# Kernel tuning notes

Hardware: AMD Instinct MI355X
Metric: run time of the kernel (lower is better)

The kernel has to match this reference:

```python
import jax, jax.numpy as jnp
import numpy as np
from jax import lax

STRIDE = 16
SCALES = (8.0, 16.0, 32.0)
RATIOS = (0.5, 1.0, 2.0)
PRE_NMS = 6000
POST_NMS = 300
NMS_THRESH = 0.7
MIN_SIZE = 16.0
DN = ('NCHW', 'OIHW', 'NCHW')


def _base_anchors():
    # 9 base anchors centered at (STRIDE/2, STRIDE/2), (ymin,xmin,ymax,xmax)
    c = STRIDE / 2.0
    rows = []
    for r in RATIOS:
        for s in SCALES:
            h = STRIDE * s * np.sqrt(r)
            w = STRIDE * s * np.sqrt(1.0 / r)
            rows.append([c - h / 2, c - w / 2, c + h / 2, c + w / 2])
    return jnp.asarray(np.array(rows, np.float32))


def _all_anchors(wdim, hdim):
    # shift base anchors over the (w, h) feature grid, matching permute(0,2,3,1) flatten order
    sy = jnp.arange(wdim, dtype=jnp.float32) * STRIDE
    sx = jnp.arange(hdim, dtype=jnp.float32) * STRIDE
    yy, xx = jnp.meshgrid(sy, sx, indexing='ij')
    shifts = jnp.stack([yy, xx, yy, xx], axis=-1).reshape(-1, 4)  # [w*h, 4]
    return (shifts[:, None, :] + _base_anchors()[None, :, :]).reshape(-1, 4)  # [w*h*9, 4]


def _conv(x, W, b, pad):
    y = lax.conv_general_dilated(x, W, (1, 1), pad, dimension_numbers=DN)
    return y + b[None, :, None, None]


def _nms_fixed(boxes, keep):
    # sequential greedy NMS over score-sorted boxes; returns POST_NMS boxes (zero padded)
    y1, x1, y2, x2 = boxes[:, 0], boxes[:, 1], boxes[:, 2], boxes[:, 3]
    areas = (y2 - y1) * (x2 - x1)
    N = boxes.shape[0]
    idxs = jnp.arange(N)

    def body(i, keep):
        yy1 = jnp.maximum(y1[i], y1)
        xx1 = jnp.maximum(x1[i], x1)
        yy2 = jnp.minimum(y2[i], y2)
        xx2 = jnp.minimum(x2[i], x2)
        inter = jnp.maximum(yy2 - yy1, 0.0) * jnp.maximum(xx2 - xx1, 0.0)
        iou = inter / (areas[i] + areas - inter + 1e-12)
        suppress = (iou > NMS_THRESH) & (idxs > i) & keep[i]
        return keep & ~suppress

    keep = lax.fori_loop(0, N, body, keep)
    rank = jnp.cumsum(keep) - 1
    slot = jnp.where(keep & (rank < POST_NMS), rank, POST_NMS)  # overflow slot
    out = jnp.zeros((POST_NMS + 1, 4), boxes.dtype).at[slot].set(boxes)
    return out[:POST_NMS]


def _proposals(loc, score_fg, anchors, img_h, img_w):
    ah = anchors[:, 2] - anchors[:, 0]
    aw = anchors[:, 3] - anchors[:, 1]
    acy = anchors[:, 0] + 0.5 * ah
    acx = anchors[:, 1] + 0.5 * aw
    cy = loc[:, 0] * ah + acy
    cx = loc[:, 1] * aw + acx
    h = jnp.exp(loc[:, 2]) * ah
    w = jnp.exp(loc[:, 3]) * aw
    boxes = jnp.stack([cy - 0.5 * h, cx - 0.5 * w, cy + 0.5 * h, cx + 0.5 * w], axis=-1)
    hi = jnp.array([img_h, img_w, img_h, img_w], dtype=boxes.dtype)
    boxes = jnp.clip(boxes, 0.0, hi)
    hs = boxes[:, 2] - boxes[:, 0]
    ws = boxes[:, 3] - boxes[:, 1]
    valid = (hs >= MIN_SIZE) & (ws >= MIN_SIZE)
    sc = jnp.where(valid, score_fg, -jnp.inf)
    top_sc, top_idx = lax.top_k(sc, PRE_NMS)
    cand = boxes[top_idx]
    return _nms_fixed(cand, jnp.isfinite(top_sc))


def setup_inputs() -> dict:
    key = jax.random.key(0)
    k = jax.random.split(key, 4)
    return {
        'base_feature_map': jax.random.normal(k[0], (8, 512, 50, 50), jnp.float32),
        'W_conv': jax.random.normal(k[1], (512, 512, 3, 3), jnp.float32) * 0.01,
        'b_conv': jnp.zeros((512,), jnp.float32),
        'W_cls': jax.random.normal(k[2], (18, 512, 1, 1), jnp.float32) * 0.01,
        'b_cls': jnp.zeros((18,), jnp.float32),
        'W_reg': jax.random.normal(k[3], (36, 512, 1, 1), jnp.float32) * 0.01,
        'b_reg': jnp.zeros((36,), jnp.float32),
        'img_h': 800,
        'img_w': 800,
    }


def reference(base_feature_map, W_conv, b_conv, W_cls, b_cls, W_reg, b_reg, img_h, img_w):
    n, _, w, h = base_feature_map.shape
    anchors = _all_anchors(w, h)  # [w*h*9, 4]
    x = jax.nn.relu(_conv(base_feature_map, W_conv, b_conv, 'SAME'))
    rpn_locs = _conv(x, W_reg, b_reg, 'VALID').transpose(0, 2, 3, 1).reshape(n, -1, 4)
    rpn_scores = _conv(x, W_cls, b_cls, 'VALID').transpose(0, 2, 3, 1).reshape(n, -1, 2)
    fg = jax.nn.softmax(rpn_scores[0], axis=-1)[:, 1]
    rois = _proposals(rpn_locs[0], fg, anchors, float(img_h), float(img_w))
    return rpn_locs, rpn_scores, anchors, rois
```

## Files before the change

### kernel.cpp

```cpp
#include <hip/hip_runtime.h>
#include <cstdint>
#include <math.h>

typedef unsigned int u32;
typedef unsigned long long u64;
typedef __attribute__((ext_vector_type(8))) short short8v;
typedef __attribute__((ext_vector_type(4))) float f32x4;

#define N_BATCH 8
#define C_IN    512
#define PX      2500
#define KDIM    4608
#define NA      22500
#define PRE_NMS 6000
#define POST_NMS 300

#define OUT_SCORES 720000
#define OUT_ANCH   1080000
#define OUT_ROIS   1170000

#define WS_X     0
#define WS_SCORE 10240000
#define WS_BOX   10262500
#define WS_WP    10388608
#define WS_XP    12747904
#define WS_END   22987904

#define NW_ELEMS (512 * KDIM)
#define NX_ELEMS (N_BATCH * C_IN * PX)

__device__ inline u32 rne_hi16(float f) {
    u32 u = __float_as_uint(f);
    return (u + 0x7FFFu + ((u >> 16) & 1u)) >> 16;
}
__device__ inline u32 pack_split(float f) {
    u32 rh  = rne_hi16(f);
    float d = f - __uint_as_float(rh << 16);
    u32 rl  = rne_hi16(d);
    return (rh << 16) | rl;
}

__global__ __launch_bounds__(256) void k_prep(const float* __restrict__ Wc,
                                              const float* __restrict__ in,
                                              u32* __restrict__ WP,
                                              u32* __restrict__ XP) {
    int o = blockIdx.x * 256 + threadIdx.x;
    if (o < NW_ELEMS) {
        int ci_in = o & 31;
        int tmp   = o >> 5;
        int r     = tmp % 9;
        int cc    = tmp / 9;
        int co    = cc >> 4;
        int cig   = cc & 15;
        int ci    = cig * 32 + ci_in;
        WP[o] = pack_split(Wc[(size_t)co * KDIM + ci * 9 + r]);
    } else {
        int o2 = o - NW_ELEMS;
        if (o2 < NX_ELEMS && XP) XP[o2] = pack_split(in[o2]);
    }
}

__global__ __launch_bounds__(256) void k_conv3(const float* __restrict__ in,
                                               const u32* __restrict__ XP,
                                               const u32* __restrict__ WP,
                                               const float* __restrict__ bc,
                                               float* __restrict__ xout) {
    __shared__ unsigned short AsH[128][40];
    __shared__ unsigned short AsL[128][40];
    __shared__ unsigned short BsH[128][40];
    __shared__ unsigned short BsL[128][40];

    int b  = blockIdx.x;
    int n  = b & 7;
    int q  = b >> 3;
    int cb = q & 3;
    int pt = q >> 2;
    int t  = threadIdx.x;
    int lane = t & 63;
    int w  = t >> 6;
    int wr = w >> 1, wc = w & 1;
    int px0 = pt * 128, co0 = cb * 128;
    const float* inN = in + (size_t)n * C_IN * PX;
    const u32*   XPn = XP ? (XP + (size_t)n * C_IN * PX) : nullptr;

    int sco = t >> 1;
    int skb = (t & 1) << 4;
    int spx = t & 127;
    int skk = (t >> 7) << 4;
    int gpx = px0 + spx;
    int sy  = gpx / 50;
    int sx  = gpx - sy * 50;
    bool pxok = (gpx < PX);
    const u32* wpA = WP + (size_t)(co0 + sco) * KDIM + skb;

    f32x4 acc[4][4];
#pragma unroll
    for (int i = 0; i < 4; ++i)
#pragma unroll
        for (int j = 0; j < 4; ++j) acc[i][j] = (f32x4)0.f;

    const int ro = lane & 15;
    const int g8 = (lane >> 4) << 3;

    for (int cig = 0; cig < 16; ++cig) {
        int ci0 = cig << 5;
        for (int r = 0; r < 9; ++r) {
            int kstep = cig * 9 + r;
            {
                const u32* wp = wpA + kstep * 32;
                u32 uu[16];
                *(uint4*)&uu[0]  = *(const uint4*)(wp);
                *(uint4*)&uu[4]  = *(const uint4*)(wp + 4);
                *(uint4*)&uu[8]  = *(const uint4*)(wp + 8);
                *(uint4*)&uu[12] = *(const uint4*)(wp + 12);
                short8v v0, v1, u0, u1;
#pragma unroll
                for (int e = 0; e < 8; ++e) {
                    v0[e] = (short)(uu[e] >> 16);
                    v1[e] = (short)(uu[8 + e] >> 16);
                    u0[e] = (short)(uu[e] & 0xFFFFu);
                    u1[e] = (short)(uu[8 + e] & 0xFFFFu);
                }
                *(short8v*)&AsH[sco][skb]     = v0;
                *(short8v*)&AsH[sco][skb + 8] = v1;
                *(short8v*)&AsL[sco][skb]     = u0;
                *(short8v*)&AsL[sco][skb + 8] = u1;
            }
            {
                int ry = (r * 11) >> 5;
                int dy = ry - 1;
                int dx = r - ry * 3 - 1;
                int iy = sy + dy, ix = sx + dx;
                bool valid = pxok && ((unsigned)iy < 50u) && ((unsigned)ix < 50u);
                int off = iy * 50 + ix;
                short8v v0, v1, u0, u1;
                if (XPn) {
                    const u32* bp = XPn + (size_t)(ci0 + skk) * PX + off;
                    u32 uu[16];
#pragma unroll
                    for (int it = 0; it < 16; ++it)
                        uu[it] = valid ? bp[it * PX] : 0u;
#pragma unroll
                    for (int e = 0; e < 8; ++e) {
                        v0[e] = (short)(uu[e] >> 16);
                        v1[e] = (short)(uu[8 + e] >> 16);
                        u0[e] = (short)(uu[e] & 0xFFFFu);
                        u1[e] = (short)(uu[8 + e] & 0xFFFFu);
                    }
                } else {
                    const float* bp = inN + (size_t)(ci0 + skk) * PX + off;
                    float bv[16];
#pragma unroll
                    for (int it = 0; it < 16; ++it)
                        bv[it] = valid ? bp[it * PX] : 0.f;
#pragma unroll
                    for (int e = 0; e < 8; ++e) {
                        u32 pa = pack_split(bv[e]);
                        u32 pb = pack_split(bv[8 + e]);
                        v0[e] = (short)(pa >> 16);
                        v1[e] = (short)(pb >> 16);
                        u0[e] = (short)(pa & 0xFFFFu);
                        u1[e] = (short)(pb & 0xFFFFu);
                    }
                }
                *(short8v*)&BsH[spx][skk]     = v0;
                *(short8v*)&BsH[spx][skk + 8] = v1;
                *(short8v*)&BsL[spx][skk]     = u0;
                *(short8v*)&BsL[spx][skk + 8] = u1;
            }
            __syncthreads();

            short8v aH[4], aL[4], bH[4], bL[4];
#pragma unroll
            for (int s = 0; s < 4; ++s) {
                aH[s] = *(const short8v*)&AsH[wr * 64 + s * 16 + ro][g8];
                aL[s] = *(const short8v*)&AsL[wr * 64 + s * 16 + ro][g8];
                bH[s] = *(const short8v*)&BsH[wc * 64 + s * 16 + ro][g8];
                bL[s] = *(const short8v*)&BsL[wc * 64 + s * 16 + ro][g8];
            }
#pragma unroll
            for (int i = 0; i < 4; ++i)
#pragma unroll
                for (int j = 0; j < 4; ++j) {
                    acc[i][j] = __builtin_amdgcn_mfma_f32_16x16x32_bf16(aH[i], bH[j], acc[i][j], 0, 0, 0);
                    acc[i][j] = __builtin_amdgcn_mfma_f32_16x16x32_bf16(aH[i], bL[j], acc[i][j], 0, 0, 0);
                    acc[i][j] = __builtin_amdgcn_mfma_f32_16x16x32_bf16(aL[i], bH[j], acc[i][j], 0, 0, 0);
                }
            __syncthreads();
        }
    }

    int coB  = co0 + wr * 64;
    int pxB  = px0 + wc * 64 + ro;
    int rowg = (lane >> 4) << 2;
#pragma unroll
    for (int i = 0; i < 4; ++i) {
#pragma unroll
        for (int rg = 0; rg < 4; ++rg) {
            int co = coB + i * 16 + rowg + rg;
            float bias = bc[co];
            float* dst = xout + ((size_t)n * C_IN + co) * PX;
#pragma unroll
            for (int j = 0; j < 4; ++j) {
                int px = pxB + j * 16;
                if (px < PX) dst[px] = fmaxf(acc[i][j][rg] + bias, 0.f);
            }
        }
    }
}

__device__ inline float readDim(const void* p) {
    int v = *(const int*)p;
    if (v > 0 && v <= 100000) return (float)v;
    return *(const float*)p;
}

__global__ __launch_bounds__(256) void k_heads(const float* __restrict__ x,
                                               const float* __restrict__ Wreg,
                                               const float* __restrict__ breg,
                                               const float* __restrict__ Wcls,
                                               const float* __restrict__ bcls,
                                               float* __restrict__ out,
                                               float* __restrict__ wsScore,
                                               float* __restrict__ wsBox,
                                               const void* pih, const void* piw) {
    __shared__ float As[32][68];
    __shared__ float Bs[32][132];
    __shared__ float Hs[54][132];
    int b  = blockIdx.x;
    int pt = b % 20, n = b / 20;
    int t  = threadIdx.x;
    int tx = t & 15, ty = t >> 4;
    int px0 = pt * 128;
    float acc[4][8];
#pragma unroll
    for (int i = 0; i < 4; ++i)
#pragma unroll
        for (int j = 0; j < 8; ++j) acc[i][j] = 0.f;

    for (int k0 = 0; k0 < 512; k0 += 32) {
        {
            int c   = t >> 2;
            int kkb = (t & 3) << 3;
            const float* src = nullptr;
            if (c < 36)      src = Wreg + (size_t)c * 512 + k0 + kkb;
            else if (c < 54) src = Wcls + (size_t)(c - 36) * 512 + k0 + kkb;
#pragma unroll
            for (int qq = 0; qq < 2; ++qq) {
                float4 wv = src ? *(const float4*)(src + qq * 4) : make_float4(0, 0, 0, 0);
                As[kkb + qq * 4 + 0][c] = wv.x;
                As[kkb + qq * 4 + 1][c] = wv.y;
                As[kkb + qq * 4 + 2][c] = wv.z;
                As[kkb + qq * 4 + 3][c] = wv.w;
            }
        }
        {
            int pxl = t & 127;
            int kk0 = (t >> 7) << 4;
            int px  = px0 + pxl;
#pragma unroll
            for (int it = 0; it < 16; ++it) {
                int kk = kk0 + it;
                float v = 0.f;
                if (px < PX) v = x[((size_t)n * 512 + k0 + kk) * PX + px];
                Bs[kk][pxl] = v;
            }
        }
        __syncthreads();
#pragma unroll 8
        for (int kk = 0; kk < 32; ++kk) {
            float a[4], bb[8];
            *(float4*)&a[0]  = *(const float4*)&As[kk][ty * 4];
            *(float4*)&bb[0] = *(const float4*)&Bs[kk][tx * 8];
            *(float4*)&bb[4] = *(const float4*)&Bs[kk][tx * 8 + 4];
#pragma unroll
            for (int i = 0; i < 4; ++i)
#pragma unroll
                for (int j = 0; j < 8; ++j)
                    acc[i][j] = fmaf(a[i], bb[j], acc[i][j]);
        }
        __syncthreads();
    }
    int pxb = px0 + tx * 8;
#pragma unroll
    for (int i = 0; i < 4; ++i) {
        int c = ty * 4 + i;
        if (c >= 54) continue;
        float bias = (c < 36) ? breg[c] : bcls[c - 36];
        for (int j = 0; j < 8; ++j) {
            int px = pxb + j;
            if (px >= PX) break;
            float v = acc[i][j] + bias;
            if (c < 36)
                out[(size_t)n * 90000 + (size_t)px * 36 + c] = v;
            else
                out[OUT_SCORES + (size_t)n * 45000 + (size_t)px * 18 + (c - 36)] = v;
            if (n == 0) Hs[c][tx * 8 + j] = v;
        }
    }

    if (n == 0) {
        __syncthreads();
        float imgH = readDim(pih), imgW = readDim(piw);
        const float ratios[3] = {0.5f, 1.f, 2.f};
        const float scales[3] = {8.f, 16.f, 32.f};
        for (int idx = t; idx < 128 * 9; idx += 256) {
            int pxl = idx / 9;
            int a   = idx - pxl * 9;
            int px  = px0 + pxl;
            if (px >= PX) continue;
            int gi = px * 9 + a;
            int y = px / 50, xq = px - y * 50;
            float r = ratios[a / 3], s = scales[a % 3];
            float hh = 16.f * s * sqrtf(r);
            float wv = 16.f * s * sqrtf(1.f / r);
            float ay1 = y * 16.f + 8.f - 0.5f * hh;
            float ax1 = xq * 16.f + 8.f - 0.5f * wv;
            float ay2 = y * 16.f + 8.f + 0.5f * hh;
            float ax2 = xq * 16.f + 8.f + 0.5f * wv;
            *(float4*)(out + OUT_ANCH + (size_t)gi * 4) = make_float4(ay1, ax1, ay2, ax2);

            float l0 = Hs[a * 4 + 0][pxl];
            float l1 = Hs[a * 4 + 1][pxl];
            float l2 = Hs[a * 4 + 2][pxl];
            float l3 = Hs[a * 4 + 3][pxl];
            float s0 = Hs[36 + 2 * a][pxl];
            float s1 = Hs[37 + 2 * a][pxl];
            float fg = 1.f / (1.f + expf(s0 - s1));
            float ah = ay2 - ay1, aw = ax2 - ax1;
            float acy = ay1 + 0.5f * ah, acx = ax1 + 0.5f * aw;
            float cy = l0 * ah + acy;
            float cx = l1 * aw + acx;
            float bh = expf(l2) * ah;
            float bw = expf(l3) * aw;
            float b0 = cy - 0.5f * bh, b1 = cx - 0.5f * bw;
            float b2 = cy + 0.5f * bh, b3 = cx + 0.5f * bw;
            b0 = fminf(fmaxf(b0, 0.f), imgH);
            b1 = fminf(fmaxf(b1, 0.f), imgW);
            b2 = fminf(fmaxf(b2, 0.f), imgH);
            b3 = fminf(fmaxf(b3, 0.f), imgW);
            bool valid = ((b2 - b0) >= 16.f) && ((b3 - b1) >= 16.f);
            wsScore[gi] = valid ? fg : -INFINITY;
            *(float4*)(wsBox + (size_t)gi * 4) = make_float4(b0, b1, b2, b3);
        }
    }
}

__device__ inline u32 fkey(float s) {
    u32 u = __float_as_uint(s);
    return (u & 0x80000000u) ? ~u : (u | 0x80000000u);
}

__global__ __launch_bounds__(1024) void k_post(const float* __restrict__ score,
                                               const float* __restrict__ boxes,
                                               float* __restrict__ rois) {
    __shared__ u32 hist[4096];
    __shared__ u64 sb[8192];
    __shared__ float kb[POST_NMS][4];
    __shared__ u64 supArr[16];
    __shared__ int sB1, sB2, sM3, sNeed, sV;
    __shared__ u32 sT32;
    __shared__ int cHi, cTie;
    int t = threadIdx.x;
    const int NT = 1024;

    for (int i = t; i < 4096; i += NT) hist[i] = 0;
    __syncthreads();
    for (int i = t; i < NA; i += NT) atomicAdd(&hist[fkey(score[i]) >> 20], 1u);
    __syncthreads();
    for (int off = 1; off < 4096; off <<= 1) {
        u32 v[4]; int c = 0;
        for (int bb = t; bb < 4096; bb += NT) { v[c++] = hist[bb] + ((bb + off < 4096) ? hist[bb + off] : 0u); }
        __syncthreads();
        c = 0;
        for (int bb = t; bb < 4096; bb += NT) hist[bb] = v[c++];
        __syncthreads();
    }
    for (int bb = t; bb < 4096; bb += NT) {
        u32 Sb  = hist[bb];
        u32 Sb1 = (bb < 4095) ? hist[bb + 1] : 0u;
        if (Sb >= PRE_NMS && Sb1 < PRE_NMS) sB1 = bb;
    }
    if (t == 0) sV = (int)hist[2048];
    __syncthreads();
    int B1 = sB1;
    int m1 = (B1 < 4095) ? (int)hist[B1 + 1] : 0;
    int V  = sV;
    __syncthreads();

    for (int i = t; i < 4096; i += NT) hist[i] = 0;
    __syncthreads();
    for (int i = t; i < NA; i += NT) {
        u32 key = fkey(score[i]);
        if ((int)(key >> 20) == B1) atomicAdd(&hist[(key >> 8) & 0xFFFu], 1u);
    }
    __syncthreads();
    for (int off = 1; off < 4096; off <<= 1) {
        u32 v[4]; int c = 0;
        for (int bb = t; bb < 4096; bb += NT) { v[c++] = hist[bb] + ((bb + off < 4096) ? hist[bb + off] : 0u); }
        __syncthreads();
        c = 0;
        for (int bb = t; bb < 4096; bb += NT) hist[bb] = v[c++];
        __syncthreads();
    }
    for (int bb = t; bb < 4096; bb += NT) {
        int Sb  = m1 + (int)hist[bb];
        int Sb1 = m1 + (int)((bb < 4095) ? hist[bb + 1] : 0u);
        if (Sb >= PRE_NMS && Sb1 < PRE_NMS) sB2 = bb;
    }
    __syncthreads();
    int B2 = sB2;
    int m2 = m1 + (int)((B2 < 4095) ? hist[B2 + 1] : 0u);
    u32 P24 = ((u32)B1 << 12) | (u32)B2;
    __syncthreads();

    for (int i = t; i < 256; i += NT) hist[i] = 0;
    __syncthreads();
    for (int i = t; i < NA; i += NT) {
        u32 key = fkey(score[i]);
        if ((key >> 8) == P24) atomicAdd(&hist[key & 0xFFu], 1u);
    }
    __syncthreads();
    for (int off = 1; off < 256; off <<= 1) {
        u32 v[1]; int c = 0;
        for (int bb = t; bb < 256; bb += NT) { v[c++] = hist[bb] + ((bb + off < 256) ? hist[bb + off] : 0u); }
        __syncthreads();
        c = 0;
        for (int bb = t; bb < 256; bb += NT) hist[bb] = v[c++];
        __syncthreads();
    }
    for (int bb = t; bb < 256; bb += NT) {
        int Sb  = m2 + (int)hist[bb];
        int Sb1 = m2 + (int)((bb < 255) ? hist[bb + 1] : 0u);
        if (Sb >= PRE_NMS && Sb1 < PRE_NMS) {
            sM3   = m2 + (int)((bb < 255) ? hist[bb + 1] : 0u);
            sNeed = PRE_NMS - sM3;
            sT32  = (P24 << 8) | (u32)bb;
        }
    }
    if (t == 0) { cHi = 0; cTie = 0; }
    __syncthreads();
    int m3 = sM3, need = sNeed;
    u32 T32 = sT32;

    for (int i = t; i < NA; i += NT) {
        u32 key = fkey(score[i]);
        u64 comp = ((u64)key << 32) | (u64)(0xFFFFFFFFu - (u32)i);
        if (key > T32) {
            int p = atomicAdd(&cHi, 1);
            sb[p] = comp;
        } else if (key == T32) {
            int p = atomicAdd(&cTie, 1);
            if (p < need) sb[m3 + p] = comp;
        }
    }
    for (int i = PRE_NMS + t; i < 8192; i += NT) sb[i] = 0ull;
    __syncthreads();

    for (int k = 2; k <= 8192; k <<= 1) {
        for (int j = k >> 1; j > 0; j >>= 1) {
            for (int i = t; i < 8192; i += NT) {
                int ixj = i ^ j;
                if (ixj > i) {
                    u64 a = sb[i], bbv = sb[ixj];
                    bool desc = ((i & k) == 0);
                    if (desc ? (a < bbv) : (a > bbv)) { sb[i] = bbv; sb[ixj] = a; }
                }
            }
            __syncthreads();
        }
    }

    int lane = t & 63, wid = t >> 6;
    int keepN = (V < PRE_NMS) ? V : PRE_NMS;
    int kept = 0;

    for (int c0 = 0; c0 < PRE_NMS && kept < POST_NMS; c0 += 64) {
        int i = c0 + lane;
        float y1 = 0, x1 = 0, y2 = 0, x2 = 0;
        bool elig = (i < keepN);
        {
            u32 bidx = 0xFFFFFFFFu - (u32)sb[i];
            float4 bx = *(const float4*)(boxes + (size_t)bidx * 4);
            y1 = bx.x; x1 = bx.y; y2 = bx.z; x2 = bx.w;
        }
        float area = (y2 - y1) * (x2 - x1);

        bool supA = false;
        for (int jj = wid; jj < kept; jj += 16) {
            float ky1 = kb[jj][0], kx1 = kb[jj][1], ky2 = kb[jj][2], kx2 = kb[jj][3];
            float yy1 = fmaxf(ky1, y1), xx1 = fmaxf(kx1, x1);
            float yy2 = fminf(ky2, y2), xx2 = fminf(kx2, x2);
            float inter = fmaxf(yy2 - yy1, 0.f) * fmaxf(xx2 - xx1, 0.f);
            float karea = (ky2 - ky1) * (kx2 - kx1);
            float iou = inter / (karea + area - inter + 1e-12f);
            if (iou > 0.7f) { supA = true; break; }
        }
        supArr[wid] = __ballot(supA);
        __syncthreads();
        u64 sup = 0ull;
#pragma unroll
        for (int ww = 0; ww < 16; ++ww) sup |= supArr[ww];
        u64 eligMask = __ballot(elig);

        for (int s = 0; s < 64; ++s) {
            if (kept >= POST_NMS) break;
            if (!((eligMask >> s) & 1ull)) continue;
            if ((sup >> s) & 1ull) continue;
            float sy1 = __shfl(y1, s), sx1 = __shfl(x1, s);
            float sy2 = __shfl(y2, s), sx2 = __shfl(x2, s);
            float sar = __shfl(area, s);
            if (wid == 0 && lane == s) {
                kb[kept][0] = y1; kb[kept][1] = x1; kb[kept][2] = y2; kb[kept][3] = x2;
                *(float4*)(rois + (size_t)kept * 4) = make_float4(y1, x1, y2, x2);
            }
            float yy1 = fmaxf(sy1, y1), xx1 = fmaxf(sx1, x1);
            float yy2 = fminf(sy2, y2), xx2 = fminf(sx2, x2);
            float inter = fmaxf(yy2 - yy1, 0.f) * fmaxf(xx2 - xx1, 0.f);
            float iou = inter / (sar + area - inter + 1e-12f);
            bool kill = (lane > s) && (iou > 0.7f);
            sup |= __ballot(kill);
            kept++;
        }
        __syncthreads();
    }
    for (int r = kept * 4 + t; r < POST_NMS * 4; r += NT) rois[r] = 0.f;
}

extern "C" void kernel_launch(void* const* d_in, const int* in_sizes, int n_in,
                              void* d_out, int out_size, void* d_ws, size_t ws_size,
                              hipStream_t stream) {
    const float* feat = (const float*)d_in[0];
    const float* Wc   = (const float*)d_in[1];
    const float* bc   = (const float*)d_in[2];
    const float* Wcls = (const float*)d_in[3];
    const float* bcls = (const float*)d_in[4];
    const float* Wreg = (const float*)d_in[5];
    const float* breg = (const float*)d_in[6];
    const void* pih   = d_in[7];
    const void* piw   = d_in[8];
    float* out = (float*)d_out;
    float* ws  = (float*)d_ws;

    u32* WP = (u32*)(ws + WS_WP);
    bool haveXP = (ws_size >= (size_t)WS_END * sizeof(float));
    u32* XP = haveXP ? (u32*)(ws + WS_XP) : nullptr;

    int prepItems = NW_ELEMS + (haveXP ? NX_ELEMS : 0);
    hipLaunchKernelGGL(k_prep, dim3((prepItems + 255) / 256), dim3(256), 0, stream, Wc, feat, WP, XP);
    hipLaunchKernelGGL(k_conv3, dim3(640), dim3(256), 0, stream, feat, XP, WP, bc, ws + WS_X);
    hipLaunchKernelGGL(k_heads, dim3(160), dim3(256), 0, stream, ws + WS_X, Wreg, breg, Wcls, bcls,
                       out, ws + WS_SCORE, ws + WS_BOX, pih, piw);
    hipLaunchKernelGGL(k_post, dim3(1), dim3(1024), 0, stream, ws + WS_SCORE, ws + WS_BOX, out + OUT_ROIS);
}
```

Baseline: 737.3 us.

## Split post-processing into select, parallel block presort, and merge+NMS kernels

The single-block post kernel is split into three launches. Top-k selection writes candidates to a global list, eight blocks bitonic-sort 1024-element chunks in parallel, and a final single block runs only the remaining merge stages before NMS. NMS now builds an intra-chunk 64x64 suppression bitmask in parallel across all 1024 threads and leaves only a cheap serial bitmask scan to thread 0, replacing the per-candidate wave shuffle loop. The cost is two extra kernel launches and a round trip of the list through global memory.

```diff
diff --git a/kernel.cpp b/kernel.cpp
--- a/kernel.cpp
+++ b/kernel.cpp
@@ -22,6 +22,8 @@
 #define WS_X     0
 #define WS_SCORE 10240000
 #define WS_BOX   10262500
+#define WS_LIST  10352500
+#define WS_META  10388500
 #define WS_WP    10388608
 #define WS_XP    12747904
 #define WS_END   22987904
@@ -351,13 +353,10 @@
     return (u & 0x80000000u) ? ~u : (u | 0x80000000u);
 }
 
-__global__ __launch_bounds__(1024) void k_post(const float* __restrict__ score,
-                                               const float* __restrict__ boxes,
-                                               float* __restrict__ rois) {
+__global__ __launch_bounds__(1024) void k_select(const float* __restrict__ score,
+                                                 u64* __restrict__ list,
+                                                 int* __restrict__ meta) {
     __shared__ u32 hist[4096];
-    __shared__ u64 sb[8192];
-    __shared__ float kb[POST_NMS][4];
-    __shared__ u64 supArr[16];
     __shared__ int sB1, sB2, sM3, sNeed, sV;
     __shared__ u32 sT32;
     __shared__ int cHi, cTie;
@@ -438,7 +437,7 @@
             sT32  = (P24 << 8) | (u32)bb;
         }
     }
-    if (t == 0) { cHi = 0; cTie = 0; }
+    if (t == 0) { cHi = 0; cTie = 0; meta[0] = (V < PRE_NMS) ? V : PRE_NMS; }
     __syncthreads();
     int m3 = sM3, need = sNeed;
     u32 T32 = sT32;
@@ -448,83 +447,135 @@
         u64 comp = ((u64)key << 32) | (u64)(0xFFFFFFFFu - (u32)i);
         if (key > T32) {
             int p = atomicAdd(&cHi, 1);
-            sb[p] = comp;
+            list[p] = comp;
         } else if (key == T32) {
             int p = atomicAdd(&cTie, 1);
-            if (p < need) sb[m3 + p] = comp;
-        }
-    }
-    for (int i = PRE_NMS + t; i < 8192; i += NT) sb[i] = 0ull;
-    __syncthreads();
-
-    for (int k = 2; k <= 8192; k <<= 1) {
+            if (p < need) list[m3 + p] = comp;
+        }
+    }
+    for (int i = PRE_NMS + t; i < 8192; i += NT) list[i] = 0ull;
+}
+
+__global__ __launch_bounds__(1024) void k_presort(u64* __restrict__ list) {
+    __shared__ u64 ls[1024];
+    int t  = threadIdx.x;
+    int gi = (blockIdx.x << 10) + t;
+    ls[t] = list[gi];
+    __syncthreads();
+    for (int k = 2; k <= 1024; k <<= 1) {
+        for (int j = k >> 1; j > 0; j >>= 1) {
+            int ixj = t ^ j;
+            if (ixj > t) {
+                u64 a = ls[t], b = ls[ixj];
+                bool desc = ((gi & k) == 0);
+                if (desc ? (a < b) : (a > b)) { ls[t] = b; ls[ixj] = a; }
+            }
+            __syncthreads();
+        }
+    }
+    list[gi] = ls[t];
+}
+
+__global__ __launch_bounds__(1024) void k_mergenms(const u64* __restrict__ list,
+                                                   const float* __restrict__ boxes,
+                                                   const int* __restrict__ meta,
+                                                   float* __restrict__ rois) {
+    __shared__ u64 sb[8192];
+    __shared__ float kb[POST_NMS][4];
+    __shared__ float cb4[64][4];
+    __shared__ u32 KLo[64], KHi[64], supA[64];
+    __shared__ int sKept;
+    int t = threadIdx.x;
+    const int NT = 1024;
+
+    for (int i = t; i < 8192; i += NT) sb[i] = list[i];
+    __syncthreads();
+
+    for (int k = 2048; k <= 8192; k <<= 1) {
         for (int j = k >> 1; j > 0; j >>= 1) {
             for (int i = t; i < 8192; i += NT) {
                 int ixj = i ^ j;
                 if (ixj > i) {
-                    u64 a = sb[i], bbv = sb[ixj];
+                    u64 a = sb[i], bv = sb[ixj];
                     bool desc = ((i & k) == 0);
-                    if (desc ? (a < bbv) : (a > bbv)) { sb[i] = bbv; sb[ixj] = a; }
+                    if (desc ? (a < bv) : (a > bv)) { sb[i] = bv; sb[ixj] = a; }
                 }
             }
             __syncthreads();
         }
     }
 
-    int lane = t & 63, wid = t >> 6;
-    int keepN = (V < PRE_NMS) ? V : PRE_NMS;
-    int kept = 0;
-
-    for (int c0 = 0; c0 < PRE_NMS && kept < POST_NMS; c0 += 64) {
-        int i = c0 + lane;
-        float y1 = 0, x1 = 0, y2 = 0, x2 = 0;
-        bool elig = (i < keepN);
-        {
-            u32 bidx = 0xFFFFFFFFu - (u32)sb[i];
+    int keepN = meta[0];
+    if (t == 0) sKept = 0;
+    __syncthreads();
+
+    int s = t >> 4, g = t & 15;
+    for (int c0 = 0; c0 < PRE_NMS; c0 += 64) {
+        if (sKept >= POST_NMS) break;
+        if (t < 64) {
+            u32 bidx = 0xFFFFFFFFu - (u32)sb[c0 + t];
+            if (bidx >= NA) bidx = 0;
             float4 bx = *(const float4*)(boxes + (size_t)bidx * 4);
-            y1 = bx.x; x1 = bx.y; y2 = bx.z; x2 = bx.w;
-        }
+            cb4[t][0] = bx.x; cb4[t][1] = bx.y; cb4[t][2] = bx.z; cb4[t][3] = bx.w;
+            KLo[t] = 0; KHi[t] = 0; supA[t] = 0;
+        }
+        __syncthreads();
+
+        float y1 = cb4[s][0], x1 = cb4[s][1], y2 = cb4[s][2], x2 = cb4[s][3];
         float area = (y2 - y1) * (x2 - x1);
 
-        bool supA = false;
-        for (int jj = wid; jj < kept; jj += 16) {
+        u32 klo = 0, khi = 0;
+#pragma unroll
+        for (int qq = 0; qq < 4; ++qq) {
+            int j = g * 4 + qq;
+            if (j > s) {
+                float jy1 = cb4[j][0], jx1 = cb4[j][1], jy2 = cb4[j][2], jx2 = cb4[j][3];
+                float yy1 = fmaxf(y1, jy1), xx1 = fmaxf(x1, jx1);
+                float yy2 = fminf(y2, jy2), xx2 = fminf(x2, jx2);
+                float inter = fmaxf(yy2 - yy1, 0.f) * fmaxf(xx2 - xx1, 0.f);
+                float ja = (jy2 - jy1) * (jx2 - jx1);
+                float iou = inter / (area + ja - inter + 1e-12f);
+                if (iou > 0.7f) { if (j < 32) klo |= 1u << j; else khi |= 1u << (j - 32); }
+            }
+        }
+        if (klo) atomicOr(&KLo[s], klo);
+        if (khi) atomicOr(&KHi[s], khi);
+
+        int kept0 = sKept;
+        bool supf = false;
+        for (int jj = g; jj < kept0; jj += 16) {
             float ky1 = kb[jj][0], kx1 = kb[jj][1], ky2 = kb[jj][2], kx2 = kb[jj][3];
             float yy1 = fmaxf(ky1, y1), xx1 = fmaxf(kx1, x1);
             float yy2 = fminf(ky2, y2), xx2 = fminf(kx2, x2);
             float inter = fmaxf(yy2 - yy1, 0.f) * fmaxf(xx2 - xx1, 0.f);
             float karea = (ky2 - ky1) * (kx2 - kx1);
             float iou = inter / (karea + area - inter + 1e-12f);
-            if (iou > 0.7f) { supA = true; break; }
-        }
-        supArr[wid] = __ballot(supA);
-        __syncthreads();
-        u64 sup = 0ull;
-#pragma unroll
-        for (int ww = 0; ww < 16; ++ww) sup |= supArr[ww];
-        u64 eligMask = __ballot(elig);
-
-        for (int s = 0; s < 64; ++s) {
-            if (kept >= POST_NMS) break;
-            if (!((eligMask >> s) & 1ull)) continue;
-            if ((sup >> s) & 1ull) continue;
-            float sy1 = __shfl(y1, s), sx1 = __shfl(x1, s);
-            float sy2 = __shfl(y2, s), sx2 = __shfl(x2, s);
-            float sar = __shfl(area, s);
-            if (wid == 0 && lane == s) {
-                kb[kept][0] = y1; kb[kept][1] = x1; kb[kept][2] = y2; kb[kept][3] = x2;
-                *(float4*)(rois + (size_t)kept * 4) = make_float4(y1, x1, y2, x2);
-            }
-            float yy1 = fmaxf(sy1, y1), xx1 = fmaxf(sx1, x1);
-            float yy2 = fminf(sy2, y2), xx2 = fminf(sx2, x2);
-            float inter = fmaxf(yy2 - yy1, 0.f) * fmaxf(xx2 - xx1, 0.f);
-            float iou = inter / (sar + area - inter + 1e-12f);
-            bool kill = (lane > s) && (iou > 0.7f);
-            sup |= __ballot(kill);
-            kept++;
-        }
-        __syncthreads();
-    }
-    for (int r = kept * 4 + t; r < POST_NMS * 4; r += NT) rois[r] = 0.f;
+            if (iou > 0.7f) { supf = true; break; }
+        }
+        if (supf) atomicOr(&supA[s], 1u);
+        __syncthreads();
+
+        if (t == 0) {
+            u64 supm = 0;
+            int kept = sKept;
+            for (int s2 = 0; s2 < 64 && kept < POST_NMS; ++s2) {
+                if (c0 + s2 >= keepN) continue;
+                if (supA[s2]) continue;
+                if ((supm >> s2) & 1ull) continue;
+                kb[kept][0] = cb4[s2][0]; kb[kept][1] = cb4[s2][1];
+                kb[kept][2] = cb4[s2][2]; kb[kept][3] = cb4[s2][3];
+                *(float4*)(rois + (size_t)kept * 4) =
+                    make_float4(cb4[s2][0], cb4[s2][1], cb4[s2][2], cb4[s2][3]);
+                kept++;
+                supm |= ((u64)KHi[s2] << 32) | (u64)KLo[s2];
+            }
+            sKept = kept;
+        }
+        __syncthreads();
+    }
+
+    int kf = sKept;
+    for (int r = kf * 4 + t; r < POST_NMS * 4; r += NT) rois[r] = 0.f;
 }
 
 extern "C" void kernel_launch(void* const* d_in, const int* in_sizes, int n_in,
@@ -542,7 +593,9 @@
     float* out = (float*)d_out;
     float* ws  = (float*)d_ws;
 
-    u32* WP = (u32*)(ws + WS_WP);
+    u32* WP   = (u32*)(ws + WS_WP);
+    u64* list = (u64*)(ws + WS_LIST);
+    int* meta = (int*)(ws + WS_META);
     bool haveXP = (ws_size >= (size_t)WS_END * sizeof(float));
     u32* XP = haveXP ? (u32*)(ws + WS_XP) : nullptr;
 
@@ -551,5 +604,7 @@
     hipLaunchKernelGGL(k_conv3, dim3(640), dim3(256), 0, stream, feat, XP, WP, bc, ws + WS_X);
     hipLaunchKernelGGL(k_heads, dim3(160), dim3(256), 0, stream, ws + WS_X, Wreg, breg, Wcls, bcls,
                        out, ws + WS_SCORE, ws + WS_BOX, pih, piw);
-    hipLaunchKernelGGL(k_post, dim3(1), dim3(1024), 0, stream, ws + WS_SCORE, ws + WS_BOX, out + OUT_ROIS);
-}
+    hipLaunchKernelGGL(k_select, dim3(1), dim3(1024), 0, stream, ws + WS_SCORE, list, meta);
+    hipLaunchKernelGGL(k_presort, dim3(8), dim3(1024), 0, stream, list);
+    hipLaunchKernelGGL(k_mergenms, dim3(1), dim3(1024), 0, stream, list, ws + WS_BOX, meta, out + OUT_ROIS);
+}
```

Measured after the change: 635.1 us. -13.9%, faster.
